# Kernel optimization log

Measured on AMD Instinct MI355X. Metric: run time of the kernel, lower is better.

The kernel has to match this reference:

```python
import jax, jax.numpy as jnp
import numpy as np

EPS = 1e-5

def setup_inputs() -> dict:
    key = jax.random.key(0)
    ks = jax.random.split(key, 5)
    B, C_clip, Hc, Wc = 8, 768, 24, 24
    C_rs, Hr, Wr = 256, 64, 64
    clip_feat = jax.random.normal(ks[0], (B, C_clip, Hc, Wc), dtype=jnp.float32)
    rs_feat = jax.random.normal(ks[1], (B, C_rs, Hr, Wr), dtype=jnp.float32)
    ln_gamma = jnp.ones((C_clip,), dtype=jnp.float32)
    ln_beta = jnp.zeros((C_clip,), dtype=jnp.float32)
    W = jax.random.normal(ks[2], (C_rs, C_clip), dtype=jnp.float32) * (1.0 / np.sqrt(C_clip))
    b = jax.random.normal(ks[3], (C_rs,), dtype=jnp.float32) * 0.01
    alpha = jnp.array([0.5], dtype=jnp.float32)
    return {"clip_feat": clip_feat, "rs_feat": rs_feat, "ln_gamma": ln_gamma,
            "ln_beta": ln_beta, "W": W, "b": b, "alpha": alpha}

def reference(clip_feat, rs_feat, ln_gamma, ln_beta, W, b, alpha):
    B, C_clip, Hc, Wc = clip_feat.shape
    _, C_rs, Hr, Wr = rs_feat.shape
    # tokens: [B, N_clip, C_clip]
    clip_flat = clip_feat.reshape(B, C_clip, Hc * Wc).transpose(0, 2, 1)
    mu = jnp.mean(clip_flat, axis=-1, keepdims=True)
    var = jnp.var(clip_flat, axis=-1, keepdims=True)
    clip_norm = (clip_flat - mu) * jax.lax.rsqrt(var + EPS) * ln_gamma + ln_beta
    # projection to rs_dim: [B, N_clip, C_rs]
    clip_proj = jnp.einsum('bnc,dc->bnd', clip_norm, W) + b
    # rs tokens: [B, N_rs, C_rs]
    rs_flat = rs_feat.reshape(B, C_rs, Hr * Wr).transpose(0, 2, 1)
    # attn_map: [B, N_clip, N_rs], softmax over N_clip (axis=1)
    attn = jnp.einsum('bnd,bmd->bnm', clip_proj, rs_flat)
    attn = jax.nn.softmax(attn, axis=1)
    # attended: [B, N_rs, C_rs]
    attended = jnp.einsum('bnm,bnd->bmd', attn, clip_proj)
    attended = attended.transpose(0, 2, 1).reshape(B, C_rs, Hr, Wr)
    return rs_feat + alpha * attended
```

## Files before the change

### kernel.cpp

```cpp
#include <hip/hip_runtime.h>
#include <hip/hip_bf16.h>

#define EPSF 1e-5f
#define SM_OFF 60.0f

typedef short short8 __attribute__((ext_vector_type(8)));
typedef float f32x4 __attribute__((ext_vector_type(4)));

__device__ __forceinline__ short f2bf(float x) {
    __hip_bfloat16 h = __float2bfloat16(x);
    return reinterpret_cast<short&>(h);
}
__device__ __forceinline__ float bf2f(short s) {
    __hip_bfloat16 h = reinterpret_cast<__hip_bfloat16&>(s);
    return __bfloat162float(h);
}
__device__ __forceinline__ unsigned int pk2(float lo, float hi) {
    return (unsigned int)(unsigned short)f2bf(lo)
         | ((unsigned int)(unsigned short)f2bf(hi) << 16);
}
__device__ __forceinline__ void gload_lds16(const short* g, short* lds) {
    __builtin_amdgcn_global_load_lds(
        (const __attribute__((address_space(1))) unsigned int*)g,
        (__attribute__((address_space(3))) unsigned int*)lds,
        16, 0, 0);
}

__global__ __launch_bounds__(256) void w_pack_kernel(
    const float* __restrict__ W,
    short* __restrict__ Wp_hi,
    short* __restrict__ Wp_lo)
{
    int t = blockIdx.x * 256 + threadIdx.x;
    int l15 = t & 15;
    int g   = (t >> 4) & 3;
    int kt  = (t >> 6) % 24;
    int nt  = t / 1536;
    const float* src = W + (size_t)(16 * nt + l15) * 768 + 32 * kt + 8 * g;
    short8 h8, l8;
    #pragma unroll
    for (int j = 0; j < 8; ++j) {
        float w = src[j];
        short h = f2bf(w);
        h8[j] = h;
        l8[j] = f2bf(w - bf2f(h));
    }
    *reinterpret_cast<short8*>(Wp_hi + (size_t)t * 8) = h8;
    *reinterpret_cast<short8*>(Wp_lo + (size_t)t * 8) = l8;
}

__global__ __launch_bounds__(512) void ln_proj_kernel(
    const float* __restrict__ clip,
    const float* __restrict__ gamma,
    const float* __restrict__ beta,
    const short* __restrict__ Wp_hi,
    const short* __restrict__ Wp_lo,
    const float* __restrict__ bias,
    short* __restrict__ proj,
    short* __restrict__ projT)
{
    __shared__ short xh[16][776];
    __shared__ short xl[16][776];
    __shared__ float redA[8][16];
    __shared__ float redB[8][16];
    __shared__ float muS[16], rsS[16];

    const int tid = threadIdx.x;
    const int bb = blockIdx.x >> 1;
    const int dh = blockIdx.x & 1;
    const int b  = bb / 36;
    const int n0 = (bb % 36) * 16;
    const int nl = tid & 15;
    const int cg = tid >> 4;
    const int w  = tid >> 6;
    const int l  = tid & 63;
    const int l15 = l & 15;
    const int g  = l >> 4;

    const float* base = clip + (size_t)b * 768 * 576 + n0 + nl;

    float x[24];
    float s1 = 0.f, s2 = 0.f;
    #pragma unroll
    for (int i = 0; i < 24; ++i) {
        x[i] = base[(size_t)(cg + 32 * i) * 576];
        s1 += x[i]; s2 += x[i] * x[i];
    }
    s1 += __shfl_xor(s1, 16); s2 += __shfl_xor(s2, 16);
    s1 += __shfl_xor(s1, 32); s2 += __shfl_xor(s2, 32);
    if (g == 0) { redA[w][l15] = s1; redB[w][l15] = s2; }
    __syncthreads();
    if (tid < 16) {
        float a = 0.f, q = 0.f;
        #pragma unroll
        for (int k = 0; k < 8; ++k) { a += redA[k][tid]; q += redB[k][tid]; }
        float mu = a * (1.f / 768.f);
        float var = q * (1.f / 768.f) - mu * mu;
        muS[tid] = mu; rsS[tid] = rsqrtf(var + EPSF);
    }
    __syncthreads();
    {
        float mu = muS[nl], rsg = rsS[nl];
        #pragma unroll
        for (int i = 0; i < 24; ++i) {
            int c = cg + 32 * i;
            float y = (x[i] - mu) * rsg * gamma[c] + beta[c];
            short hh = f2bf(y);
            xh[nl][c] = hh;
            xl[nl][c] = f2bf(y - bf2f(hh));
        }
    }
    __syncthreads();

    const int nt = 8 * dh + w;
    f32x4 acc = f32x4{0.f, 0.f, 0.f, 0.f};
    for (int kt = 0; kt < 24; ++kt) {
        short8 ah = *reinterpret_cast<const short8*>(&xh[l15][32 * kt + 8 * g]);
        short8 al = *reinterpret_cast<const short8*>(&xl[l15][32 * kt + 8 * g]);
        size_t off = ((size_t)((nt * 24 + kt) * 64 + l)) * 8;
        short8 bh = *reinterpret_cast<const short8*>(Wp_hi + off);
        short8 bl = *reinterpret_cast<const short8*>(Wp_lo + off);
        acc = __builtin_amdgcn_mfma_f32_16x16x32_bf16(ah, bh, acc, 0, 0, 0);
        acc = __builtin_amdgcn_mfma_f32_16x16x32_bf16(al, bh, acc, 0, 0, 0);
        acc = __builtin_amdgcn_mfma_f32_16x16x32_bf16(ah, bl, acc, 0, 0, 0);
    }

    {
        int d = 16 * nt + l15;
        float bb2 = bias[d];
        #pragma unroll
        for (int r = 0; r < 4; ++r) {
            int tok = n0 + 4 * g + r;
            short v = f2bf(acc[r] + bb2);
            proj[((size_t)b * 576 + tok) * 256 + d] = v;
            projT[((size_t)b * 256 + d) * 576 + tok] = v;
        }
    }
}

__global__ __launch_bounds__(256, 2) void attn_kernel(
    const short* __restrict__ proj,
    const short* __restrict__ projT,
    const float* __restrict__ rs,
    const float* __restrict__ alpha_p,
    float* __restrict__ out)
{
    __shared__ short Ks[2][32][256];
    __shared__ short VT[2][256][32];
    __shared__ unsigned int Ps[4][16][20];

    const int tid = threadIdx.x;
    const int b  = blockIdx.x >> 6;
    const int q0 = (blockIdx.x & 63) << 6;
    const int w   = tid >> 6;
    const int l   = tid & 63;
    const int l15 = l & 15;
    const int g   = l >> 4;
    const int qg  = q0 + 16 * w + l15;

    const short* kbase  = proj  + (size_t)b * 576 * 256;
    const short* ktbase = projT + (size_t)b * 256 * 576;
    const float* rbase  = rs + (size_t)b * 256 * 4096;
    float* obase = out + (size_t)b * 256 * 4096;

    short8 qf[8];
    #pragma unroll
    for (int dc = 0; dc < 8; ++dc) {
        short8 v;
        #pragma unroll
        for (int j = 0; j < 8; ++j)
            v[j] = f2bf(rbase[(size_t)(32 * dc + 8 * g + j) * 4096 + qg]);
        qf[dc] = v;
    }

    f32x4 acc[16];
    #pragma unroll
    for (int dt = 0; dt < 16; ++dt) acc[dt] = f32x4{0.f, 0.f, 0.f, 0.f};
    float rsum = 0.f;

    auto STAGE = [&](int c, int buf) {
        #pragma unroll
        for (int i = 0; i < 4; ++i) {
            int rr = 8 * w + 2 * i + (l >> 5);
            const short* src = kbase + ((size_t)(32 * c + rr) << 8)
                             + ((((l & 31) ^ (rr & 7))) << 3);
            gload_lds16(src, &Ks[buf][8 * w + 2 * i][0]);
        }
        #pragma unroll
        for (int i = 0; i < 4; ++i) {
            int d = 64 * w + 16 * i + (l >> 2);
            const short* src = ktbase + (size_t)d * 576 + 32 * c + 8 * (l & 3);
            gload_lds16(src, &VT[buf][64 * w + 16 * i][0]);
        }
    };

    STAGE(0, 0);
    __syncthreads();

    for (int c = 0; c < 18; ++c) {
        const int cur = c & 1;
        if (c < 17) STAGE(c + 1, cur ^ 1);

        f32x4 s0{0.f,0.f,0.f,0.f}, s1{0.f,0.f,0.f,0.f};
        __builtin_amdgcn_s_setprio(1);
        #pragma unroll
        for (int dc = 0; dc < 8; ++dc) {
            int sw = (((4 * dc + g) ^ (l15 & 7))) * 8;
            short8 kf0 = *reinterpret_cast<const short8*>(&Ks[cur][l15][sw]);
            short8 kf1 = *reinterpret_cast<const short8*>(&Ks[cur][16 + l15][sw]);
            s0 = __builtin_amdgcn_mfma_f32_16x16x32_bf16(kf0, qf[dc], s0, 0, 0, 0);
            s1 = __builtin_amdgcn_mfma_f32_16x16x32_bf16(kf1, qf[dc], s1, 0, 0, 0);
        }
        __builtin_amdgcn_s_setprio(0);

        float p[8];
        #pragma unroll
        for (int r = 0; r < 4; ++r) {
            p[r]     = __expf(s0[r] - SM_OFF);
            p[4 + r] = __expf(s1[r] - SM_OFF);
        }
        #pragma unroll
        for (int r = 0; r < 8; ++r) rsum += p[r];

        unsigned int u0 = pk2(p[0], p[1]), u1 = pk2(p[2], p[3]);
        unsigned int u2 = pk2(p[4], p[5]), u3 = pk2(p[6], p[7]);
        *reinterpret_cast<uint2*>(&Ps[w][l15][2 * g])     = uint2{u0, u1};
        *reinterpret_cast<uint2*>(&Ps[w][l15][8 + 2 * g]) = uint2{u2, u3};

        short8 pf = *reinterpret_cast<const short8*>(&Ps[w][l15][4 * g]);
        __builtin_amdgcn_s_setprio(1);
        #pragma unroll
        for (int dt = 0; dt < 16; ++dt) {
            short8 vf = *reinterpret_cast<const short8*>(&VT[cur][16 * dt + l15][8 * g]);
            acc[dt] = __builtin_amdgcn_mfma_f32_16x16x32_bf16(vf, pf, acc[dt], 0, 0, 0);
        }
        __builtin_amdgcn_s_setprio(0);

        if (c < 17) __syncthreads();
    }

    rsum += __shfl_xor(rsum, 16);
    rsum += __shfl_xor(rsum, 32);
    float inv = alpha_p[0] / rsum;

    #pragma unroll
    for (int dt = 0; dt < 16; ++dt) {
        #pragma unroll
        for (int r = 0; r < 4; ++r) {
            int d = 16 * dt + 4 * g + r;
            size_t idx = (size_t)d * 4096 + qg;
            obase[idx] = rbase[idx] + acc[dt][r] * inv;
        }
    }
}

extern "C" void kernel_launch(void* const* d_in, const int* in_sizes, int n_in,
                              void* d_out, int out_size, void* d_ws, size_t ws_size,
                              hipStream_t stream)
{
    const float* clip  = (const float*)d_in[0];
    const float* rsf   = (const float*)d_in[1];
    const float* gamma = (const float*)d_in[2];
    const float* beta  = (const float*)d_in[3];
    const float* W     = (const float*)d_in[4];
    const float* bias  = (const float*)d_in[5];
    const float* alpha = (const float*)d_in[6];
    float* out = (float*)d_out;

    char* ws = (char*)d_ws;
    short* Wp_hi = (short*)ws;
    short* Wp_lo = (short*)(ws + 393216);
    short* proj  = (short*)(ws + 786432);
    short* projT = (short*)(ws + 3145728);

    hipLaunchKernelGGL(w_pack_kernel, dim3(96), dim3(256), 0, stream, W, Wp_hi, Wp_lo);
    hipLaunchKernelGGL(ln_proj_kernel, dim3(576), dim3(512), 0, stream,
                       clip, gamma, beta, Wp_hi, Wp_lo, bias, proj, projT);
    hipLaunchKernelGGL(attn_kernel, dim3(512), dim3(256), 0, stream,
                       proj, projT, rsf, alpha, out);
}
```

Before: 72.32 us.

## Split attention waves by query pair and key/D half to reuse LDS fragments

Each wave now covers two 16-query tiles but only half of each 32-key chunk for the scores, and only half of the 256 output channels for the PV product. Each K and V^T fragment read from LDS now feeds two MFMAs instead of one, roughly halving LDS read traffic per MFMA. The price is cross-wave sharing: probabilities go through a double-buffered LDS buffer behind an extra barrier each chunk, and row sums are combined through LDS at the end. The next-chunk prefetch is also moved after that barrier, so it starts later in each iteration.

```diff
diff --git a/kernel.cpp b/kernel.cpp
--- a/kernel.cpp
+++ b/kernel.cpp
@@ -147,7 +147,8 @@
 {
     __shared__ short Ks[2][32][256];
     __shared__ short VT[2][256][32];
-    __shared__ unsigned int Ps[4][16][20];
+    __shared__ unsigned int Pb[2][2][2][16][20];
+    __shared__ float Rb[2][2][2][16];
 
     const int tid = threadIdx.x;
     const int b  = blockIdx.x >> 6;
@@ -156,27 +157,35 @@
     const int l   = tid & 63;
     const int l15 = l & 15;
     const int g   = l >> 4;
-    const int qg  = q0 + 16 * w + l15;
+    const int qh  = w >> 1;
+    const int kh  = w & 1;
+    const int qb  = q0 + 32 * qh;
 
     const short* kbase  = proj  + (size_t)b * 576 * 256;
     const short* ktbase = projT + (size_t)b * 256 * 576;
     const float* rbase  = rs + (size_t)b * 256 * 4096;
     float* obase = out + (size_t)b * 256 * 4096;
 
-    short8 qf[8];
-    #pragma unroll
-    for (int dc = 0; dc < 8; ++dc) {
-        short8 v;
-        #pragma unroll
-        for (int j = 0; j < 8; ++j)
-            v[j] = f2bf(rbase[(size_t)(32 * dc + 8 * g + j) * 4096 + qg]);
-        qf[dc] = v;
-    }
-
-    f32x4 acc[16];
-    #pragma unroll
-    for (int dt = 0; dt < 16; ++dt) acc[dt] = f32x4{0.f, 0.f, 0.f, 0.f};
-    float rsum = 0.f;
+    short8 qf[2][8];
+    #pragma unroll
+    for (int qt = 0; qt < 2; ++qt) {
+        int qg = qb + 16 * qt + l15;
+        #pragma unroll
+        for (int dc = 0; dc < 8; ++dc) {
+            short8 v;
+            #pragma unroll
+            for (int j = 0; j < 8; ++j)
+                v[j] = f2bf(rbase[(size_t)(32 * dc + 8 * g + j) * 4096 + qg]);
+            qf[qt][dc] = v;
+        }
+    }
+
+    f32x4 acc[2][8];
+    #pragma unroll
+    for (int qt = 0; qt < 2; ++qt)
+        #pragma unroll
+        for (int dt = 0; dt < 8; ++dt) acc[qt][dt] = f32x4{0.f, 0.f, 0.f, 0.f};
+    float rsum[2] = {0.f, 0.f};
 
     auto STAGE = [&](int c, int buf) {
         #pragma unroll
@@ -199,57 +208,75 @@
 
     for (int c = 0; c < 18; ++c) {
         const int cur = c & 1;
-        if (c < 17) STAGE(c + 1, cur ^ 1);
 
         f32x4 s0{0.f,0.f,0.f,0.f}, s1{0.f,0.f,0.f,0.f};
         __builtin_amdgcn_s_setprio(1);
         #pragma unroll
         for (int dc = 0; dc < 8; ++dc) {
             int sw = (((4 * dc + g) ^ (l15 & 7))) * 8;
-            short8 kf0 = *reinterpret_cast<const short8*>(&Ks[cur][l15][sw]);
-            short8 kf1 = *reinterpret_cast<const short8*>(&Ks[cur][16 + l15][sw]);
-            s0 = __builtin_amdgcn_mfma_f32_16x16x32_bf16(kf0, qf[dc], s0, 0, 0, 0);
-            s1 = __builtin_amdgcn_mfma_f32_16x16x32_bf16(kf1, qf[dc], s1, 0, 0, 0);
+            short8 kf = *reinterpret_cast<const short8*>(&Ks[cur][16 * kh + l15][sw]);
+            s0 = __builtin_amdgcn_mfma_f32_16x16x32_bf16(kf, qf[0][dc], s0, 0, 0, 0);
+            s1 = __builtin_amdgcn_mfma_f32_16x16x32_bf16(kf, qf[1][dc], s1, 0, 0, 0);
         }
         __builtin_amdgcn_s_setprio(0);
 
-        float p[8];
+        float p0[4], p1[4];
         #pragma unroll
         for (int r = 0; r < 4; ++r) {
-            p[r]     = __expf(s0[r] - SM_OFF);
-            p[4 + r] = __expf(s1[r] - SM_OFF);
-        }
-        #pragma unroll
-        for (int r = 0; r < 8; ++r) rsum += p[r];
-
-        unsigned int u0 = pk2(p[0], p[1]), u1 = pk2(p[2], p[3]);
-        unsigned int u2 = pk2(p[4], p[5]), u3 = pk2(p[6], p[7]);
-        *reinterpret_cast<uint2*>(&Ps[w][l15][2 * g])     = uint2{u0, u1};
-        *reinterpret_cast<uint2*>(&Ps[w][l15][8 + 2 * g]) = uint2{u2, u3};
-
-        short8 pf = *reinterpret_cast<const short8*>(&Ps[w][l15][4 * g]);
+            p0[r] = __expf(s0[r] - SM_OFF);
+            p1[r] = __expf(s1[r] - SM_OFF);
+            rsum[0] += p0[r]; rsum[1] += p1[r];
+        }
+        *reinterpret_cast<uint2*>(&Pb[cur][qh][0][l15][8 * kh + 2 * g]) =
+            uint2{pk2(p0[0], p0[1]), pk2(p0[2], p0[3])};
+        *reinterpret_cast<uint2*>(&Pb[cur][qh][1][l15][8 * kh + 2 * g]) =
+            uint2{pk2(p1[0], p1[1]), pk2(p1[2], p1[3])};
+
+        __syncthreads();
+
+        if (c < 17) STAGE(c + 1, cur ^ 1);
+
+        short8 pf0 = *reinterpret_cast<const short8*>(&Pb[cur][qh][0][l15][4 * g]);
+        short8 pf1 = *reinterpret_cast<const short8*>(&Pb[cur][qh][1][l15][4 * g]);
         __builtin_amdgcn_s_setprio(1);
         #pragma unroll
-        for (int dt = 0; dt < 16; ++dt) {
-            short8 vf = *reinterpret_cast<const short8*>(&VT[cur][16 * dt + l15][8 * g]);
-            acc[dt] = __builtin_amdgcn_mfma_f32_16x16x32_bf16(vf, pf, acc[dt], 0, 0, 0);
+        for (int dt = 0; dt < 8; ++dt) {
+            short8 vf = *reinterpret_cast<const short8*>(
+                &VT[cur][128 * kh + 16 * dt + l15][8 * g]);
+            acc[0][dt] = __builtin_amdgcn_mfma_f32_16x16x32_bf16(vf, pf0, acc[0][dt], 0, 0, 0);
+            acc[1][dt] = __builtin_amdgcn_mfma_f32_16x16x32_bf16(vf, pf1, acc[1][dt], 0, 0, 0);
         }
         __builtin_amdgcn_s_setprio(0);
 
         if (c < 17) __syncthreads();
     }
 
-    rsum += __shfl_xor(rsum, 16);
-    rsum += __shfl_xor(rsum, 32);
-    float inv = alpha_p[0] / rsum;
-
-    #pragma unroll
-    for (int dt = 0; dt < 16; ++dt) {
-        #pragma unroll
-        for (int r = 0; r < 4; ++r) {
-            int d = 16 * dt + 4 * g + r;
-            size_t idx = (size_t)d * 4096 + qg;
-            obase[idx] = rbase[idx] + acc[dt][r] * inv;
+    #pragma unroll
+    for (int qt = 0; qt < 2; ++qt) {
+        rsum[qt] += __shfl_xor(rsum[qt], 16);
+        rsum[qt] += __shfl_xor(rsum[qt], 32);
+    }
+    if (g == 0) {
+        Rb[qh][kh][0][l15] = rsum[0];
+        Rb[qh][kh][1][l15] = rsum[1];
+    }
+    __syncthreads();
+    float av = alpha_p[0];
+    float inv0 = av / (Rb[qh][0][0][l15] + Rb[qh][1][0][l15]);
+    float inv1 = av / (Rb[qh][0][1][l15] + Rb[qh][1][1][l15]);
+
+    #pragma unroll
+    for (int qt = 0; qt < 2; ++qt) {
+        float inv = qt ? inv1 : inv0;
+        int qg = qb + 16 * qt + l15;
+        #pragma unroll
+        for (int dt = 0; dt < 8; ++dt) {
+            #pragma unroll
+            for (int r = 0; r < 4; ++r) {
+                int d = 128 * kh + 16 * dt + 4 * g + r;
+                size_t idx = (size_t)d * 4096 + qg;
+                obase[idx] = rbase[idx] + acc[qt][dt][r] * inv;
+            }
         }
     }
 }
```

Result: no change. 72.33 us (+0.0%).

## Split attention output channels across two blocks and drop LDS double buffering

Applied to the files above, without the earlier changes.

Each attention block now computes only half of the 256 output channels, so the grid doubles to 1024 blocks. The accumulator array and V tile shrink by half, and the K/V tiles go from double- to single-buffered so more blocks fit per CU (launch bounds raised to 4). The cost is that QK^T scores and the softmax exponentials are computed twice, once per half, and the next tile load no longer overlaps compute, which adds an extra barrier per chunk.

```diff
diff --git a/kernel.cpp b/kernel.cpp
--- a/kernel.cpp
+++ b/kernel.cpp
@@ -138,20 +138,22 @@
     }
 }
 
-__global__ __launch_bounds__(256, 2) void attn_kernel(
+__global__ __launch_bounds__(256, 4) void attn_kernel(
     const short* __restrict__ proj,
     const short* __restrict__ projT,
     const float* __restrict__ rs,
     const float* __restrict__ alpha_p,
     float* __restrict__ out)
 {
-    __shared__ short Ks[2][32][256];
-    __shared__ short VT[2][256][32];
+    __shared__ short Ks[32][256];
+    __shared__ short VT[128][32];
     __shared__ unsigned int Ps[4][16][20];
 
     const int tid = threadIdx.x;
-    const int b  = blockIdx.x >> 6;
-    const int q0 = (blockIdx.x & 63) << 6;
+    const int dh = blockIdx.x & 1;
+    const int qt = (blockIdx.x >> 1) & 63;
+    const int b  = blockIdx.x >> 7;
+    const int q0 = qt << 6;
     const int w   = tid >> 6;
     const int l   = tid & 63;
     const int l15 = l & 15;
@@ -163,6 +165,25 @@
     const float* rbase  = rs + (size_t)b * 256 * 4096;
     float* obase = out + (size_t)b * 256 * 4096;
 
+    auto STAGE = [&](int c) {
+        #pragma unroll
+        for (int i = 0; i < 4; ++i) {
+            int row0 = 8 * w + 2 * i;
+            int rr = row0 + (l >> 5);
+            const short* src = kbase + ((size_t)(32 * c + rr) << 8)
+                             + ((((l & 31) ^ (rr & 7))) << 3);
+            gload_lds16(src, &Ks[row0][0]);
+        }
+        #pragma unroll
+        for (int i = 0; i < 2; ++i) {
+            int d0 = 32 * w + 16 * i;
+            int d = 128 * dh + d0 + (l >> 2);
+            const short* src = ktbase + (size_t)d * 576 + 32 * c + 8 * (l & 3);
+            gload_lds16(src, &VT[d0][0]);
+        }
+    };
+
+    STAGE(0);
     short8 qf[8];
     #pragma unroll
     for (int dc = 0; dc < 8; ++dc) {
@@ -173,41 +194,21 @@
         qf[dc] = v;
     }
 
-    f32x4 acc[16];
-    #pragma unroll
-    for (int dt = 0; dt < 16; ++dt) acc[dt] = f32x4{0.f, 0.f, 0.f, 0.f};
+    f32x4 acc[8];
+    #pragma unroll
+    for (int dt = 0; dt < 8; ++dt) acc[dt] = f32x4{0.f, 0.f, 0.f, 0.f};
     float rsum = 0.f;
 
-    auto STAGE = [&](int c, int buf) {
-        #pragma unroll
-        for (int i = 0; i < 4; ++i) {
-            int rr = 8 * w + 2 * i + (l >> 5);
-            const short* src = kbase + ((size_t)(32 * c + rr) << 8)
-                             + ((((l & 31) ^ (rr & 7))) << 3);
-            gload_lds16(src, &Ks[buf][8 * w + 2 * i][0]);
-        }
-        #pragma unroll
-        for (int i = 0; i < 4; ++i) {
-            int d = 64 * w + 16 * i + (l >> 2);
-            const short* src = ktbase + (size_t)d * 576 + 32 * c + 8 * (l & 3);
-            gload_lds16(src, &VT[buf][64 * w + 16 * i][0]);
-        }
-    };
-
-    STAGE(0, 0);
     __syncthreads();
 
     for (int c = 0; c < 18; ++c) {
-        const int cur = c & 1;
-        if (c < 17) STAGE(c + 1, cur ^ 1);
-
         f32x4 s0{0.f,0.f,0.f,0.f}, s1{0.f,0.f,0.f,0.f};
         __builtin_amdgcn_s_setprio(1);
         #pragma unroll
         for (int dc = 0; dc < 8; ++dc) {
             int sw = (((4 * dc + g) ^ (l15 & 7))) * 8;
-            short8 kf0 = *reinterpret_cast<const short8*>(&Ks[cur][l15][sw]);
-            short8 kf1 = *reinterpret_cast<const short8*>(&Ks[cur][16 + l15][sw]);
+            short8 kf0 = *reinterpret_cast<const short8*>(&Ks[l15][sw]);
+            short8 kf1 = *reinterpret_cast<const short8*>(&Ks[16 + l15][sw]);
             s0 = __builtin_amdgcn_mfma_f32_16x16x32_bf16(kf0, qf[dc], s0, 0, 0, 0);
             s1 = __builtin_amdgcn_mfma_f32_16x16x32_bf16(kf1, qf[dc], s1, 0, 0, 0);
         }
@@ -230,13 +231,17 @@
         short8 pf = *reinterpret_cast<const short8*>(&Ps[w][l15][4 * g]);
         __builtin_amdgcn_s_setprio(1);
         #pragma unroll
-        for (int dt = 0; dt < 16; ++dt) {
-            short8 vf = *reinterpret_cast<const short8*>(&VT[cur][16 * dt + l15][8 * g]);
+        for (int dt = 0; dt < 8; ++dt) {
+            short8 vf = *reinterpret_cast<const short8*>(&VT[16 * dt + l15][8 * g]);
             acc[dt] = __builtin_amdgcn_mfma_f32_16x16x32_bf16(vf, pf, acc[dt], 0, 0, 0);
         }
         __builtin_amdgcn_s_setprio(0);
 
-        if (c < 17) __syncthreads();
+        __syncthreads();
+        if (c < 17) {
+            STAGE(c + 1);
+            __syncthreads();
+        }
     }
 
     rsum += __shfl_xor(rsum, 16);
@@ -244,10 +249,10 @@
     float inv = alpha_p[0] / rsum;
 
     #pragma unroll
-    for (int dt = 0; dt < 16; ++dt) {
+    for (int dt = 0; dt < 8; ++dt) {
         #pragma unroll
         for (int r = 0; r < 4; ++r) {
-            int d = 16 * dt + 4 * g + r;
+            int d = 128 * dh + 16 * dt + 4 * g + r;
             size_t idx = (size_t)d * 4096 + qg;
             obase[idx] = rbase[idx] + acc[dt][r] * inv;
         }
@@ -276,6 +281,6 @@
     hipLaunchKernelGGL(w_pack_kernel, dim3(96), dim3(256), 0, stream, W, Wp_hi, Wp_lo);
     hipLaunchKernelGGL(ln_proj_kernel, dim3(576), dim3(512), 0, stream,
                        clip, gamma, beta, Wp_hi, Wp_lo, bias, proj, projT);
-    hipLaunchKernelGGL(attn_kernel, dim3(512), dim3(256), 0, stream,
+    hipLaunchKernelGGL(attn_kernel, dim3(1024), dim3(256), 0, stream,
                        proj, projT, rsf, alpha, out);
 }
```

Result: slower. 79.02 us (+9.3%).
